# Performance work log

Measured on AMD Instinct MI355X. Metric: run time of the kernel, lower is better.

Reference implementation:

```python
import jax, jax.numpy as jnp
import numpy as np

N_NODES = 100000
N_EDGES = 1000000
N_GRAPHS = 128
D_NODE = 64
D_EDGE = 32
D_HID = 64
D_OUT = 1


def setup_inputs() -> dict:
    key = jax.random.key(0)
    ks = jax.random.split(key, 24)

    def lin(k, fi, fo):
        s = 1.0 / np.sqrt(fi)
        kw, kb = jax.random.split(k)
        W = jax.random.uniform(kw, (fi, fo), jnp.float32, -s, s)
        b = jax.random.uniform(kb, (fo,), jnp.float32, -s, s)
        return W, b

    x = jax.random.normal(ks[0], (N_NODES, D_NODE), jnp.float32)
    edge_attr = jax.random.normal(ks[1], (N_EDGES, D_EDGE), jnp.float32)
    edge_src = jax.random.randint(ks[2], (N_EDGES,), 0, N_NODES, jnp.int32)
    edge_dst = jax.random.randint(ks[3], (N_EDGES,), 0, N_NODES, jnp.int32)
    batch = jnp.sort(jax.random.randint(ks[4], (N_NODES,), 0, N_GRAPHS, jnp.int32))

    We1, be1 = lin(ks[5], D_EDGE, D_NODE)   # conv1 edge lin: edge_dim -> in_channels
    W11, b11 = lin(ks[6], D_NODE, D_HID)    # mlp1 layer 1
    W12, b12 = lin(ks[7], D_HID, D_HID)     # mlp1 layer 2
    We2, be2 = lin(ks[8], D_EDGE, D_HID)    # conv2 edge lin
    W21, b21 = lin(ks[9], D_HID, D_HID)     # mlp2 layer 1
    W22, b22 = lin(ks[10], D_HID, D_HID)    # mlp2 layer 2
    Wf1, bf1 = lin(ks[11], D_HID, 2 * D_HID)
    Wf2, bf2 = lin(ks[12], 2 * D_HID, D_OUT)
    eps1 = jnp.zeros((), jnp.float32)  # train_eps=True, init 0
    eps2 = jnp.zeros((), jnp.float32)

    return dict(x=x, edge_attr=edge_attr, edge_src=edge_src, edge_dst=edge_dst,
                batch=batch, eps1=eps1, We1=We1, be1=be1, W11=W11, b11=b11,
                W12=W12, b12=b12, eps2=eps2, We2=We2, be2=be2, W21=W21, b21=b21,
                W22=W22, b22=b22, Wf1=Wf1, bf1=bf1, Wf2=Wf2, bf2=bf2)


def _gine_conv(x, edge_attr, edge_src, edge_dst, eps, We, be, W1, b1, W2, b2):
    # message = ReLU(x_j + lin_edge(e)); scatter-sum to dst; nn((1+eps)*x + aggr)
    e = edge_attr @ We + be                      # [E, d]
    m = jax.nn.relu(x[edge_src] + e)             # gather + fuse, [E, d]
    aggr = jax.ops.segment_sum(m, edge_dst, num_segments=N_NODES)  # [N, d]
    h = (1.0 + eps) * x + aggr
    return jax.nn.relu(h @ W1 + b1) @ W2 + b2


def reference(x, edge_attr, edge_src, edge_dst, batch, eps1, We1, be1, W11, b11,
              W12, b12, eps2, We2, be2, W21, b21, W22, b22, Wf1, bf1, Wf2, bf2):
    h = jax.nn.relu(_gine_conv(x, edge_attr, edge_src, edge_dst,
                               eps1, We1, be1, W11, b11, W12, b12))
    # dropout: eval mode (identity)
    h = jax.nn.relu(_gine_conv(h, edge_attr, edge_src, edge_dst,
                               eps2, We2, be2, W21, b21, W22, b22))
    pooled = jax.ops.segment_sum(h, batch, num_segments=N_GRAPHS)  # global_add_pool
    return jax.nn.relu(pooled @ Wf1 + bf1) @ Wf2 + bf2
```

## Files before the change

### kernel.cpp

```cpp
#include <hip/hip_runtime.h>

#define N_NODES 100000
#define N_EDGES 1000000
#define N_GRAPHS 128
#define NPW 4
#define SCAN_BLK 1024
#define SCAN_NB ((N_NODES + SCAN_BLK - 1) / SCAN_BLK)

__device__ __forceinline__ float rl(float v, int l) {
    return __uint_as_float(__builtin_amdgcn_readlane(__float_as_uint(v), l));
}

__global__ __launch_bounds__(256) void count_kernel(
    const int* __restrict__ dst, int* __restrict__ counts)
{
    int e = blockIdx.x * blockDim.x + threadIdx.x;
    if (e < N_EDGES) atomicAdd(&counts[dst[e]], 1);
}

__global__ __launch_bounds__(SCAN_BLK) void scan1_kernel(
    const int* __restrict__ counts, int* __restrict__ cursor,
    int* __restrict__ bsum)
{
    __shared__ int sm[SCAN_BLK];
    const int t = threadIdx.x;
    const int i = blockIdx.x * SCAN_BLK + t;
    const int v = (i < N_NODES) ? counts[i] : 0;
    sm[t] = v;
    __syncthreads();
    for (int off = 1; off < SCAN_BLK; off <<= 1) {
        int tmp = (t >= off) ? sm[t - off] : 0;
        __syncthreads();
        sm[t] += tmp;
        __syncthreads();
    }
    if (i < N_NODES) cursor[i] = sm[t] - v;
    if (t == SCAN_BLK - 1) bsum[blockIdx.x] = sm[t];
}

__global__ __launch_bounds__(128) void scan2_kernel(
    const int* __restrict__ bsum, int* __restrict__ boff)
{
    __shared__ int sm[128];
    const int t = threadIdx.x;
    const int v = (t < SCAN_NB) ? bsum[t] : 0;
    sm[t] = v;
    __syncthreads();
    for (int off = 1; off < 128; off <<= 1) {
        int tmp = (t >= off) ? sm[t - off] : 0;
        __syncthreads();
        sm[t] += tmp;
        __syncthreads();
    }
    if (t < SCAN_NB) boff[t] = sm[t] - v;
}

__global__ __launch_bounds__(SCAN_BLK) void scan3_kernel(
    int* __restrict__ cursor, const int* __restrict__ boff)
{
    const int i = blockIdx.x * SCAN_BLK + threadIdx.x;
    if (i < N_NODES) cursor[i] += boff[blockIdx.x];
}

__global__ __launch_bounds__(256) void pos_kernel(
    const int* __restrict__ src, const int* __restrict__ dst,
    int* __restrict__ cursor,
    int* __restrict__ pos_s, int* __restrict__ src_s)
{
    int e = blockIdx.x * blockDim.x + threadIdx.x;
    if (e >= N_EDGES) return;
    int p = atomicAdd(&cursor[dst[e]], 1);
    pos_s[e] = p;
    src_s[p] = src[e];
}

__global__ __launch_bounds__(256) void perm_kernel(
    const float* __restrict__ ea, const int* __restrict__ pos_s,
    float* __restrict__ ea_s)
{
    const int lane  = threadIdx.x & 63;
    const int wid   = (blockIdx.x * blockDim.x + threadIdx.x) >> 6;
    const int r     = lane >> 3;
    const int q     = lane & 7;
    const int ebase = wid * 8;
    if (ebase >= N_EDGES) return;

    const int mypos = pos_s[ebase + r];
    const float4 v = *(const float4*)(ea + (size_t)(ebase + r) * 32 + q * 4);
    *(float4*)(ea_s + (size_t)mypos * 32 + q * 4) = v;
}

__global__ __launch_bounds__(256) void edge_csr_kernel(
    const float* __restrict__ x,
    const float* __restrict__ ea_s,
    const int*   __restrict__ src_s,
    const int*   __restrict__ rowend,
    const float* __restrict__ We,
    const float* __restrict__ be,
    float*       __restrict__ aggr)
{
    const int lane = threadIdx.x & 63;
    const int wid  = (blockIdx.x * blockDim.x + threadIdx.x) >> 6;
    const int n0   = __builtin_amdgcn_readfirstlane(wid * NPW);
    if (n0 >= N_NODES) return;
    const int n1 = min(n0 + NPW, N_NODES);

    float w[32];
#pragma unroll
    for (int k = 0; k < 32; ++k) w[k] = We[k * 64 + lane];
    float b = be[lane];
#pragma unroll
    for (int k = 0; k < 32; ++k) asm volatile("" : "+v"(w[k]));
    asm volatile("" : "+v"(b));

    int p = (n0 == 0) ? 0 : rowend[n0 - 1];
    for (int n = n0; n < n1; ++n) {
        const int pe = rowend[n];
        float acc = 0.0f;
        for (; p + 2 <= pe; p += 2) {
            const float ev  = ea_s[(size_t)p * 32 + lane];
            const int s0 = src_s[p];
            const int s1 = src_s[p + 1];
            const float xv0 = x[(size_t)s0 * 64 + lane];
            const float xv1 = x[(size_t)s1 * 64 + lane];
            float a0 = b, a1 = 0.f, a2 = 0.f, a3 = 0.f;
            float c0 = b, c1 = 0.f, c2 = 0.f, c3 = 0.f;
#pragma unroll
            for (int k = 0; k < 32; k += 4) {
                a0 = fmaf(rl(ev, k+0),    w[k+0], a0);
                a1 = fmaf(rl(ev, k+1),    w[k+1], a1);
                a2 = fmaf(rl(ev, k+2),    w[k+2], a2);
                a3 = fmaf(rl(ev, k+3),    w[k+3], a3);
                c0 = fmaf(rl(ev, 32+k+0), w[k+0], c0);
                c1 = fmaf(rl(ev, 32+k+1), w[k+1], c1);
                c2 = fmaf(rl(ev, 32+k+2), w[k+2], c2);
                c3 = fmaf(rl(ev, 32+k+3), w[k+3], c3);
            }
            acc += fmaxf(xv0 + ((a0 + a1) + (a2 + a3)), 0.0f)
                 + fmaxf(xv1 + ((c0 + c1) + (c2 + c3)), 0.0f);
        }
        if (p < pe) {
            const float ev = ea_s[(size_t)p * 32 + (lane & 31)];
            const int s = src_s[p];
            const float xv = x[(size_t)s * 64 + lane];
            float a0 = b, a1 = 0.f, a2 = 0.f, a3 = 0.f;
#pragma unroll
            for (int k = 0; k < 32; k += 4) {
                a0 = fmaf(rl(ev, k+0), w[k+0], a0);
                a1 = fmaf(rl(ev, k+1), w[k+1], a1);
                a2 = fmaf(rl(ev, k+2), w[k+2], a2);
                a3 = fmaf(rl(ev, k+3), w[k+3], a3);
            }
            acc += fmaxf(xv + ((a0 + a1) + (a2 + a3)), 0.0f);
            ++p;
        }
        aggr[(size_t)n * 64 + lane] = acc;
    }
}

__global__ __launch_bounds__(256) void node_kernel(
    const float* __restrict__ x_in, const float* __restrict__ aggr,
    const float* __restrict__ eps,
    const float* __restrict__ W1, const float* __restrict__ b1,
    const float* __restrict__ W2, const float* __restrict__ b2,
    float* __restrict__ h_out)
{
    const int lane = threadIdx.x & 63;
    const int wid  = (blockIdx.x * blockDim.x + threadIdx.x) >> 6;
    const int nw   = (gridDim.x * blockDim.x) >> 6;

    float w1[64], w2[64];
#pragma unroll
    for (int i = 0; i < 64; ++i) w1[i] = W1[i * 64 + lane];
#pragma unroll
    for (int i = 0; i < 64; ++i) w2[i] = W2[i * 64 + lane];
#pragma unroll
    for (int i = 0; i < 64; ++i) asm volatile("" : "+v"(w1[i]));
#pragma unroll
    for (int i = 0; i < 64; ++i) asm volatile("" : "+v"(w2[i]));
    const float b1v = b1[lane];
    const float b2v = b2[lane];
    const float ep  = 1.0f + eps[0];

    for (int n = wid; n < N_NODES; n += nw) {
        const size_t base = (size_t)n * 64;
        const float h = fmaf(ep, x_in[base + lane], aggr[base + lane]);

        float t0 = b1v, t1 = 0.f, t2 = 0.f, t3 = 0.f;
#pragma unroll
        for (int i = 0; i < 64; i += 4) {
            t0 = fmaf(rl(h, i+0), w1[i+0], t0);
            t1 = fmaf(rl(h, i+1), w1[i+1], t1);
            t2 = fmaf(rl(h, i+2), w1[i+2], t2);
            t3 = fmaf(rl(h, i+3), w1[i+3], t3);
        }
        const float t = fmaxf((t0 + t1) + (t2 + t3), 0.0f);

        float o0 = b2v, o1 = 0.f, o2 = 0.f, o3 = 0.f;
#pragma unroll
        for (int i = 0; i < 64; i += 4) {
            o0 = fmaf(rl(t, i+0), w2[i+0], o0);
            o1 = fmaf(rl(t, i+1), w2[i+1], o1);
            o2 = fmaf(rl(t, i+2), w2[i+2], o2);
            o3 = fmaf(rl(t, i+3), w2[i+3], o3);
        }
        h_out[base + lane] = fmaxf((o0 + o1) + (o2 + o3), 0.0f);
    }
}

#define POOL_CHUNK 16
__global__ __launch_bounds__(256) void pool_kernel(
    const float* __restrict__ h, const int* __restrict__ batch,
    float* __restrict__ pooled)
{
    const int lane  = threadIdx.x & 63;
    const int wid   = (blockIdx.x * blockDim.x + threadIdx.x) >> 6;
    const int start = wid * POOL_CHUNK;
    if (start >= N_NODES) return;
    const int end = min(start + POOL_CHUNK, N_NODES);

    int   gcur = batch[start];
    float acc  = 0.0f;
    for (int n = start; n < end; ++n) {
        const int g = batch[n];
        if (g != gcur) {
            atomicAdd(&pooled[gcur * 64 + lane], acc);
            acc  = 0.0f;
            gcur = g;
        }
        acc += h[(size_t)n * 64 + lane];
    }
    atomicAdd(&pooled[gcur * 64 + lane], acc);
}

__global__ __launch_bounds__(128) void head_kernel(
    const float* __restrict__ pooled, const float* __restrict__ Wf1,
    const float* __restrict__ bf1, const float* __restrict__ Wf2,
    const float* __restrict__ bf2, float* __restrict__ out)
{
    __shared__ float p[64];
    __shared__ float red[2];
    const int g = blockIdx.x;
    const int j = threadIdx.x;

    if (j < 64) p[j] = pooled[g * 64 + j];
    __syncthreads();

    float t = bf1[j];
#pragma unroll
    for (int i = 0; i < 64; ++i)
        t = fmaf(p[i], Wf1[i * 128 + j], t);
    t = fmaxf(t, 0.0f);

    float v = t * Wf2[j];
    for (int off = 32; off > 0; off >>= 1)
        v += __shfl_down(v, off);
    if ((j & 63) == 0) red[j >> 6] = v;
    __syncthreads();
    if (j == 0) out[g] = red[0] + red[1] + bf2[0];
}

extern "C" void kernel_launch(void* const* d_in, const int* in_sizes, int n_in,
                              void* d_out, int out_size, void* d_ws, size_t ws_size,
                              hipStream_t stream) {
    const float* x    = (const float*)d_in[0];
    const float* ea   = (const float*)d_in[1];
    const int*   esrc = (const int*)  d_in[2];
    const int*   edst = (const int*)  d_in[3];
    const int*   batch= (const int*)  d_in[4];
    const float* eps1 = (const float*)d_in[5];
    const float* We1  = (const float*)d_in[6];
    const float* be1  = (const float*)d_in[7];
    const float* W11  = (const float*)d_in[8];
    const float* b11  = (const float*)d_in[9];
    const float* W12  = (const float*)d_in[10];
    const float* b12  = (const float*)d_in[11];
    const float* eps2 = (const float*)d_in[12];
    const float* We2  = (const float*)d_in[13];
    const float* be2  = (const float*)d_in[14];
    const float* W21  = (const float*)d_in[15];
    const float* b21  = (const float*)d_in[16];
    const float* W22  = (const float*)d_in[17];
    const float* b22  = (const float*)d_in[18];
    const float* Wf1  = (const float*)d_in[19];
    const float* bf1  = (const float*)d_in[20];
    const float* Wf2  = (const float*)d_in[21];
    const float* bf2  = (const float*)d_in[22];
    float* out = (float*)d_out;

    const size_t NF = (size_t)N_NODES * 64 * sizeof(float);
    char* ws = (char*)d_ws;
    float* aggr   = (float*)ws;
    float* h      = (float*)(ws + NF);
    float* pooled = (float*)(ws + 2 * NF);
    char*  p4     = ws + 2 * NF + 32768;
    int* counts = (int*)p4;
    int* cursor = (int*)(p4 + 409600);
    int* src_s  = (int*)(p4 + 2 * 409600);
    int* bsum   = (int*)(p4 + 2 * 409600 + 4000000);
    int* boff   = (int*)(p4 + 2 * 409600 + 4000512);
    char*  p5   = p4 + 2 * 409600 + 4001024;
    float* ea_s = (float*)p5;
    int* pos_s  = (int*)aggr;

    const int E_TH_BLOCKS  = (N_EDGES + 255) / 256;
    const int PERM_BLOCKS  = (N_EDGES / 8 + 3) / 4;
    const int EDGE_WAVES   = (N_NODES + NPW - 1) / NPW;
    const int EDGE_BLOCKS  = (EDGE_WAVES + 3) / 4;
    const int NODE_BLOCKS  = 1024;
    const int POOL_BLOCKS  = ((N_NODES + POOL_CHUNK - 1) / POOL_CHUNK + 3) / 4;

    hipMemsetAsync(counts, 0, 409600, stream);
    count_kernel<<<E_TH_BLOCKS, 256, 0, stream>>>(edst, counts);
    scan1_kernel<<<SCAN_NB, SCAN_BLK, 0, stream>>>(counts, cursor, bsum);
    scan2_kernel<<<1, 128, 0, stream>>>(bsum, boff);
    scan3_kernel<<<SCAN_NB, SCAN_BLK, 0, stream>>>(cursor, boff);
    pos_kernel<<<E_TH_BLOCKS, 256, 0, stream>>>(esrc, edst, cursor, pos_s, src_s);
    perm_kernel<<<PERM_BLOCKS, 256, 0, stream>>>(ea, pos_s, ea_s);

    edge_csr_kernel<<<EDGE_BLOCKS, 256, 0, stream>>>(
        x, ea_s, src_s, cursor, We1, be1, aggr);
    node_kernel<<<NODE_BLOCKS, 256, 0, stream>>>(x, aggr, eps1, W11, b11, W12, b12, h);

    edge_csr_kernel<<<EDGE_BLOCKS, 256, 0, stream>>>(
        h, ea_s, src_s, cursor, We2, be2, aggr);
    node_kernel<<<NODE_BLOCKS, 256, 0, stream>>>(h, aggr, eps2, W21, b21, W22, b22, h);

    hipMemsetAsync(pooled, 0, (size_t)N_GRAPHS * 64 * sizeof(float), stream);
    pool_kernel<<<POOL_BLOCKS, 256, 0, stream>>>(h, batch, pooled);
    head_kernel<<<N_GRAPHS, 128, 0, stream>>>(pooled, Wf1, bf1, Wf2, bf2, out);
}
```

Before: 710.8 us.

## Stage edge features in LDS and use packed FMA for matvecs

The edge kernel now copies tiles of 32 sorted edge-attribute rows into per-wave shared memory. Each edge's 32-element projection is computed from LDS broadcast reads with v_pk_fma_f32, replacing 32 readlane operations per edge. The node MLP kernel likewise writes h and t to shared memory and uses packed FMA instead of readlane broadcasts. The aim is to cut the scalar-readlane bottleneck and double FMA throughput per instruction. The cost is extra LDS traffic and intra-wave write-then-read ordering through shared memory without explicit barriers, which relies on wave-level execution order.

```diff
diff --git a/kernel.cpp b/kernel.cpp
--- a/kernel.cpp
+++ b/kernel.cpp
@@ -4,11 +4,17 @@
 #define N_EDGES 1000000
 #define N_GRAPHS 128
 #define NPW 4
+#define TILE_E 32
 #define SCAN_BLK 1024
 #define SCAN_NB ((N_NODES + SCAN_BLK - 1) / SCAN_BLK)
 
-__device__ __forceinline__ float rl(float v, int l) {
-    return __uint_as_float(__builtin_amdgcn_readlane(__float_as_uint(v), l));
+typedef float v2f __attribute__((ext_vector_type(2)));
+typedef float v4f __attribute__((ext_vector_type(4)));
+
+__device__ __forceinline__ v2f pk_fma(v2f a, v2f b, v2f c) {
+    v2f d;
+    asm("v_pk_fma_f32 %0, %1, %2, %3" : "=v"(d) : "v"(a), "v"(b), "v"(c));
+    return d;
 }
 
 __global__ __launch_bounds__(256) void count_kernel(
@@ -99,60 +105,64 @@
     const float* __restrict__ be,
     float*       __restrict__ aggr)
 {
-    const int lane = threadIdx.x & 63;
-    const int wid  = (blockIdx.x * blockDim.x + threadIdx.x) >> 6;
-    const int n0   = __builtin_amdgcn_readfirstlane(wid * NPW);
+    __shared__ float smem[4][TILE_E * 32];
+    const int lane  = threadIdx.x & 63;
+    const int wslot = threadIdx.x >> 6;
+    const int wid   = (blockIdx.x * blockDim.x + threadIdx.x) >> 6;
+    const int n0    = __builtin_amdgcn_readfirstlane(wid * NPW);
     if (n0 >= N_NODES) return;
     const int n1 = min(n0 + NPW, N_NODES);
 
-    float w[32];
-#pragma unroll
-    for (int k = 0; k < 32; ++k) w[k] = We[k * 64 + lane];
+    v2f w2[16];
+#pragma unroll
+    for (int k = 0; k < 16; ++k)
+        w2[k] = (v2f){We[(2 * k) * 64 + lane], We[(2 * k + 1) * 64 + lane]};
     float b = be[lane];
 #pragma unroll
-    for (int k = 0; k < 32; ++k) asm volatile("" : "+v"(w[k]));
+    for (int k = 0; k < 16; ++k) asm volatile("" : "+v"(w2[k]));
     asm volatile("" : "+v"(b));
 
+    v4f* buf4 = (v4f*)smem[wslot];
+
     int p = (n0 == 0) ? 0 : rowend[n0 - 1];
+    const int pend = rowend[n1 - 1];
+    int bufpos = TILE_E;
+
     for (int n = n0; n < n1; ++n) {
         const int pe = rowend[n];
         float acc = 0.0f;
-        for (; p + 2 <= pe; p += 2) {
-            const float ev  = ea_s[(size_t)p * 32 + lane];
-            const int s0 = src_s[p];
-            const int s1 = src_s[p + 1];
-            const float xv0 = x[(size_t)s0 * 64 + lane];
-            const float xv1 = x[(size_t)s1 * 64 + lane];
-            float a0 = b, a1 = 0.f, a2 = 0.f, a3 = 0.f;
-            float c0 = b, c1 = 0.f, c2 = 0.f, c3 = 0.f;
-#pragma unroll
-            for (int k = 0; k < 32; k += 4) {
-                a0 = fmaf(rl(ev, k+0),    w[k+0], a0);
-                a1 = fmaf(rl(ev, k+1),    w[k+1], a1);
-                a2 = fmaf(rl(ev, k+2),    w[k+2], a2);
-                a3 = fmaf(rl(ev, k+3),    w[k+3], a3);
-                c0 = fmaf(rl(ev, 32+k+0), w[k+0], c0);
-                c1 = fmaf(rl(ev, 32+k+1), w[k+1], c1);
-                c2 = fmaf(rl(ev, 32+k+2), w[k+2], c2);
-                c3 = fmaf(rl(ev, 32+k+3), w[k+3], c3);
+        for (; p < pe; ++p) {
+            if (bufpos == TILE_E) {
+                const int tn8 = min(TILE_E, pend - p) * 8;
+                const v4f* g4 = (const v4f*)(ea_s + (size_t)p * 32);
+                if (tn8 == TILE_E * 8) {
+                    v4f a0 = g4[lane], a1 = g4[lane + 64],
+                        a2 = g4[lane + 128], a3 = g4[lane + 192];
+                    buf4[lane] = a0;       buf4[lane + 64] = a1;
+                    buf4[lane + 128] = a2; buf4[lane + 192] = a3;
+                } else {
+                    for (int j = lane; j < tn8; j += 64) buf4[j] = g4[j];
+                }
+                bufpos = 0;
             }
-            acc += fmaxf(xv0 + ((a0 + a1) + (a2 + a3)), 0.0f)
-                 + fmaxf(xv1 + ((c0 + c1) + (c2 + c3)), 0.0f);
-        }
-        if (p < pe) {
-            const float ev = ea_s[(size_t)p * 32 + (lane & 31)];
             const int s = src_s[p];
             const float xv = x[(size_t)s * 64 + lane];
-            float a0 = b, a1 = 0.f, a2 = 0.f, a3 = 0.f;
-#pragma unroll
-            for (int k = 0; k < 32; k += 4) {
-                a0 = fmaf(rl(ev, k+0), w[k+0], a0);
-                a1 = fmaf(rl(ev, k+1), w[k+1], a1);
-                a2 = fmaf(rl(ev, k+2), w[k+2], a2);
-                a3 = fmaf(rl(ev, k+3), w[k+3], a3);
+
+            v2f e0 = {0.f, 0.f}, e1 = {0.f, 0.f},
+                e2 = {0.f, 0.f}, e3 = {0.f, 0.f};
+            const int bo8 = bufpos * 8;
+#pragma unroll
+            for (int j = 0; j < 8; j += 2) {
+                const v4f qa = buf4[bo8 + j];
+                const v4f qb = buf4[bo8 + j + 1];
+                e0 = pk_fma(qa.xy, w2[2 * j + 0], e0);
+                e1 = pk_fma(qa.zw, w2[2 * j + 1], e1);
+                e2 = pk_fma(qb.xy, w2[2 * j + 2], e2);
+                e3 = pk_fma(qb.zw, w2[2 * j + 3], e3);
             }
-            acc += fmaxf(xv + ((a0 + a1) + (a2 + a3)), 0.0f);
-            ++p;
+            const v2f es = (e0 + e1) + (e2 + e3);
+            acc += fmaxf(xv + (es.x + es.y + b), 0.0f);
+            ++bufpos;
         }
         aggr[(size_t)n * 64 + lane] = acc;
     }
@@ -165,46 +175,62 @@
     const float* __restrict__ W2, const float* __restrict__ b2,
     float* __restrict__ h_out)
 {
-    const int lane = threadIdx.x & 63;
-    const int wid  = (blockIdx.x * blockDim.x + threadIdx.x) >> 6;
-    const int nw   = (gridDim.x * blockDim.x) >> 6;
-
-    float w1[64], w2[64];
-#pragma unroll
-    for (int i = 0; i < 64; ++i) w1[i] = W1[i * 64 + lane];
-#pragma unroll
-    for (int i = 0; i < 64; ++i) w2[i] = W2[i * 64 + lane];
-#pragma unroll
-    for (int i = 0; i < 64; ++i) asm volatile("" : "+v"(w1[i]));
-#pragma unroll
-    for (int i = 0; i < 64; ++i) asm volatile("" : "+v"(w2[i]));
+    __shared__ float hsm[4][64];
+    __shared__ float tsm[4][64];
+    const int lane  = threadIdx.x & 63;
+    const int wslot = threadIdx.x >> 6;
+    const int wid   = (blockIdx.x * blockDim.x + threadIdx.x) >> 6;
+    const int nw    = (gridDim.x * blockDim.x) >> 6;
+
+    v2f w1p[32], w2p[32];
+#pragma unroll
+    for (int j = 0; j < 32; ++j)
+        w1p[j] = (v2f){W1[(2 * j) * 64 + lane], W1[(2 * j + 1) * 64 + lane]};
+#pragma unroll
+    for (int j = 0; j < 32; ++j)
+        w2p[j] = (v2f){W2[(2 * j) * 64 + lane], W2[(2 * j + 1) * 64 + lane]};
+#pragma unroll
+    for (int j = 0; j < 32; ++j) asm volatile("" : "+v"(w1p[j]));
+#pragma unroll
+    for (int j = 0; j < 32; ++j) asm volatile("" : "+v"(w2p[j]));
     const float b1v = b1[lane];
     const float b2v = b2[lane];
     const float ep  = 1.0f + eps[0];
 
+    const v4f* hv = (const v4f*)hsm[wslot];
+    const v4f* tv = (const v4f*)tsm[wslot];
+
     for (int n = wid; n < N_NODES; n += nw) {
         const size_t base = (size_t)n * 64;
         const float h = fmaf(ep, x_in[base + lane], aggr[base + lane]);
-
-        float t0 = b1v, t1 = 0.f, t2 = 0.f, t3 = 0.f;
-#pragma unroll
-        for (int i = 0; i < 64; i += 4) {
-            t0 = fmaf(rl(h, i+0), w1[i+0], t0);
-            t1 = fmaf(rl(h, i+1), w1[i+1], t1);
-            t2 = fmaf(rl(h, i+2), w1[i+2], t2);
-            t3 = fmaf(rl(h, i+3), w1[i+3], t3);
+        hsm[wslot][lane] = h;
+
+        v2f t0 = {0.f, 0.f}, t1 = {0.f, 0.f}, t2 = {0.f, 0.f}, t3 = {0.f, 0.f};
+#pragma unroll
+        for (int j = 0; j < 16; j += 2) {
+            const v4f qa = hv[j];
+            const v4f qb = hv[j + 1];
+            t0 = pk_fma(qa.xy, w1p[2 * j + 0], t0);
+            t1 = pk_fma(qa.zw, w1p[2 * j + 1], t1);
+            t2 = pk_fma(qb.xy, w1p[2 * j + 2], t2);
+            t3 = pk_fma(qb.zw, w1p[2 * j + 3], t3);
         }
-        const float t = fmaxf((t0 + t1) + (t2 + t3), 0.0f);
-
-        float o0 = b2v, o1 = 0.f, o2 = 0.f, o3 = 0.f;
-#pragma unroll
-        for (int i = 0; i < 64; i += 4) {
-            o0 = fmaf(rl(t, i+0), w2[i+0], o0);
-            o1 = fmaf(rl(t, i+1), w2[i+1], o1);
-            o2 = fmaf(rl(t, i+2), w2[i+2], o2);
-            o3 = fmaf(rl(t, i+3), w2[i+3], o3);
+        const v2f tsum = (t0 + t1) + (t2 + t3);
+        const float t = fmaxf(tsum.x + tsum.y + b1v, 0.0f);
+        tsm[wslot][lane] = t;
+
+        v2f o0 = {0.f, 0.f}, o1 = {0.f, 0.f}, o2 = {0.f, 0.f}, o3 = {0.f, 0.f};
+#pragma unroll
+        for (int j = 0; j < 16; j += 2) {
+            const v4f qa = tv[j];
+            const v4f qb = tv[j + 1];
+            o0 = pk_fma(qa.xy, w2p[2 * j + 0], o0);
+            o1 = pk_fma(qa.zw, w2p[2 * j + 1], o1);
+            o2 = pk_fma(qb.xy, w2p[2 * j + 2], o2);
+            o3 = pk_fma(qb.zw, w2p[2 * j + 3], o3);
         }
-        h_out[base + lane] = fmaxf((o0 + o1) + (o2 + o3), 0.0f);
+        const v2f osum = (o0 + o1) + (o2 + o3);
+        h_out[base + lane] = fmaxf(osum.x + osum.y + b2v, 0.0f);
     }
 }
 
```

Measured after the change: 667.1 us. 1.07x faster.
